# Kernel tuning notes

Measured on AMD Instinct MI355X. Metric: run time of the kernel, lower is better.

The kernel has to match this reference:

```python
import jax, jax.numpy as jnp
import numpy as np

T = 1.0          # temperature
W_PARENT = 0.3
W_CHILD = 0.7
EPS = 1e-8


def _conv(x, w, stride=1):
    # x: [N,C,H,W], w: [O,I,kh,kw]
    return jax.lax.conv_general_dilated(
        x, w, (stride, stride), 'SAME',
        dimension_numbers=('NCHW', 'OIHW', 'NCHW'))


def setup_inputs() -> dict:
    key = jax.random.key(0)
    ks = jax.random.split(key, 12)
    B, H, W = 64, 256, 256
    E, CMID = 8, 8
    GF = 64  # gating feature dim
    s = lambda k, shape, fan: jax.random.normal(k, shape, jnp.float32) * (1.0 / np.sqrt(fan))
    return {
        'x':   jax.random.normal(ks[0], (B, 1, H, W), jnp.float32),
        # gating network (frozen): conv stem + avg pool + two heads
        'Wg':  s(ks[1], (GF, 1, 7, 7), 49),
        'Wc':  s(ks[2], (6, GF), GF),
        'bc':  jnp.zeros((6,), jnp.float32),
        'Wp':  s(ks[3], (2, GF), GF),
        'bp':  jnp.zeros((2,), jnp.float32),
        # 8 experts, each a 1->CMID->1 conv stack (DIVAESR proxy)
        'We1': s(ks[4], (E, CMID, 1, 3, 3), 9),
        'be1': jnp.zeros((E, CMID), jnp.float32),
        'We2': s(ks[5], (E, 1, CMID, 3, 3), 9 * CMID),
        'be2': jnp.zeros((E, 1), jnp.float32),
    }


def _gating(x, Wg, Wc, bc, Wp, bp):
    # frozen multi-task classifier: conv stem, global avg pool, two linear heads
    h = jax.nn.relu(_conv(x, Wg, stride=4))        # [B,GF,H/4,W/4]
    feats = jnp.mean(h, axis=(2, 3))               # [B,GF]
    child_logits = (feats @ Wc.T + bc) / T         # [B,6]
    parent_logits = (feats @ Wp.T + bp) / T        # [B,2]
    child_probs = jax.nn.softmax(child_logits, axis=1)
    parent_probs = jax.nn.softmax(parent_logits, axis=1)
    parent_val = jnp.max(parent_probs, axis=1)
    parent_idx = jnp.argmax(parent_probs, axis=1)
    child_val = jnp.max(child_probs, axis=1)
    child_idx = jnp.argmax(child_probs, axis=1) + 2   # global expert id in [2,7]
    wp = W_PARENT * parent_val
    wc = W_CHILD * child_val
    tot = wp + wc + EPS
    topk_indices = jnp.stack([parent_idx, child_idx], axis=1)   # [B,2] int
    probs = jnp.stack([wp / tot, wc / tot], axis=1)             # [B,2]
    return topk_indices, probs


def _expert_single(xi, w1, b1, w2, b2):
    # xi: [1,H,W]; per-sample expert conv stack with gathered kernels
    h = jax.nn.relu(_conv(xi[None], w1) + b1[None, :, None, None])
    y = _conv(h, w2) + b2[None, :, None, None]
    return y[0]  # [1,H,W]


def _dispatch_combine(x, topk_indices, probs, We1, be1, We2, be2):
    # fused gather-dispatch / combine: gather each sample's two expert kernels
    run = jax.vmap(_expert_single)
    p_idx, c_idx = topk_indices[:, 0], topk_indices[:, 1]
    out_p = run(x, We1[p_idx], be1[p_idx], We2[p_idx], be2[p_idx])  # [B,1,H,W]
    out_c = run(x, We1[c_idx], be1[c_idx], We2[c_idx], be2[c_idx])
    return (probs[:, 0, None, None, None] * out_p
            + probs[:, 1, None, None, None] * out_c)


def reference(x, Wg, Wc, bc, Wp, bp, We1, be1, We2, be2):
    topk_indices, probs = _gating(x, Wg, Wc, bc, Wp, bp)
    return _dispatch_combine(x, topk_indices, probs, We1, be1, We2, be2)
```

## Files before the change

### kernel.cpp

```cpp
#include <hip/hip_runtime.h>
#include <hip/hip_bf16.h>
#include <math.h>

#define IMG 256

typedef __attribute__((ext_vector_type(4))) short short4v;
typedef __attribute__((ext_vector_type(8))) short short8v;
typedef __attribute__((ext_vector_type(4))) float f32x4;
typedef __attribute__((ext_vector_type(2))) float v2f;
typedef _Float16 half2v __attribute__((ext_vector_type(2)));

__device__ __forceinline__ short bf16s(float f) {
    __hip_bfloat16 h = __float2bfloat16(f);
    short s; __builtin_memcpy(&s, &h, 2); return s;
}
__device__ __forceinline__ half2v h2bits(unsigned int u) {
    half2v h; __builtin_memcpy(&h, &u, 4); return h;
}
template <typename T>
__device__ __forceinline__ unsigned int bits4(T v) {
    static_assert(sizeof(T) == 4, "bits4 needs 4-byte type");
    unsigned int u; __builtin_memcpy(&u, &v, 4); return u;
}
__device__ __forceinline__ unsigned int h16b(float f) {
    _Float16 h = (_Float16)f;
    unsigned short s; __builtin_memcpy(&s, &h, 2); return (unsigned int)s;
}

__global__ __launch_bounds__(256) void gate_mfma_kernel(
    const float* __restrict__ x, const float* __restrict__ Wg,
    const float* __restrict__ We2,
    float* __restrict__ partials, unsigned int* __restrict__ w2pack)
{
    __shared__ short xs[36 * 136];
    __shared__ float red[4][64];

    const int tile = blockIdx.x;
    const int rt = tile >> 1, ct = tile & 1;
    const int b   = blockIdx.y;
    const int tid = threadIdx.x;

    const float* xb = x + (size_t)b * (IMG * IMG);
    const int gy0 = rt * 32 - 1;
    {
        const int qx = tid & 31;
        const int rb = tid >> 5;
        #pragma unroll
        for (int t = 0; t < 5; ++t) {
            const int r = rb + 8 * t;
            if (r < 36) {
                const int gy = gy0 + r;
                float4 v = make_float4(0.f, 0.f, 0.f, 0.f);
                if (gy >= 0 && gy < IMG)
                    v = *(const float4*)&xb[gy * IMG + 128 * ct + 4 * qx];
                short* p = &xs[r * 136 + 4 * qx + 1];
                p[0] = bf16s(v.x); p[1] = bf16s(v.y); p[2] = bf16s(v.z); p[3] = bf16s(v.w);
            }
        }
    }
    if (tid < 36) {
        const int r = tid, gy = gy0 + r;
        float v = 0.f;
        if (gy >= 0 && gy < IMG && ct == 1) v = xb[gy * IMG + 127];
        xs[r * 136] = bf16s(v);
    }
    if (tid < 36) {
        const int r = tid, gy = gy0 + r;
        float4 v = make_float4(0.f, 0.f, 0.f, 0.f);
        if (gy >= 0 && gy < IMG && ct == 0)
            v = *(const float4*)&xb[gy * IMG + 128];
        short* p = &xs[r * 136 + 129];
        p[0] = bf16s(v.x); p[1] = bf16s(v.y); p[2] = bf16s(v.z); p[3] = bf16s(v.w);
    }

    const int lane = tid & 63;
    const int wv_  = tid >> 6;
    const int m    = lane & 15;
    const int kb   = lane >> 4;

    short8v Bhi[2][4], Blo[2][4];
    #pragma unroll
    for (int s = 0; s < 2; ++s) {
        const int ky = kb + 4 * s;
        #pragma unroll
        for (int nc = 0; nc < 4; ++nc) {
            const int gf = nc * 16 + m;
            short8v bh, bl;
            #pragma unroll
            for (int j = 0; j < 8; ++j) {
                float wv = 0.f;
                if (j < 7 && ky < 7) wv = Wg[gf * 49 + ky * 7 + j];
                const short hi = bf16s(wv);
                const float hif = __uint_as_float(((unsigned int)(unsigned short)hi) << 16);
                bh[j] = hi;
                bl[j] = bf16s(wv - hif);
            }
            Bhi[s][nc] = bh; Blo[s][nc] = bl;
        }
    }

    __syncthreads();

    float rsum[4] = {0.f, 0.f, 0.f, 0.f};
    const f32x4 zero4 = {0.f, 0.f, 0.f, 0.f};

    #pragma unroll 1
    for (int i = 0; i < 4; ++i) {
        const int chunk = wv_ * 4 + i;
        const int r = chunk >> 1, q = chunk & 1;
        short8v A[2];
        #pragma unroll
        for (int s = 0; s < 2; ++s) {
            const int row = 4 * r + kb + 4 * s;
            const short4v* p = (const short4v*)&xs[row * 136 + 64 * q + 4 * m];
            const short4v lo4 = p[0], hi4 = p[1];
            A[s] = __builtin_shufflevector(lo4, hi4, 0, 1, 2, 3, 4, 5, 6, 7);
        }
        #pragma unroll
        for (int nc = 0; nc < 4; ++nc) {
            f32x4 z = __builtin_amdgcn_mfma_f32_16x16x32_bf16(A[0], Bhi[0][nc], zero4, 0, 0, 0);
            z = __builtin_amdgcn_mfma_f32_16x16x32_bf16(A[1], Bhi[1][nc], z, 0, 0, 0);
            z = __builtin_amdgcn_mfma_f32_16x16x32_bf16(A[0], Blo[0][nc], z, 0, 0, 0);
            z = __builtin_amdgcn_mfma_f32_16x16x32_bf16(A[1], Blo[1][nc], z, 0, 0, 0);
            rsum[nc] += fmaxf(z[0], 0.f) + fmaxf(z[1], 0.f) + fmaxf(z[2], 0.f) + fmaxf(z[3], 0.f);
        }
    }

    #pragma unroll
    for (int nc = 0; nc < 4; ++nc) {
        float v = rsum[nc];
        v += __shfl_xor(v, 16);
        v += __shfl_xor(v, 32);
        if (lane < 16) red[wv_][nc * 16 + lane] = v;
    }
    __syncthreads();
    if (tid < 64) {
        const float s = red[0][tid] + red[1][tid] + red[2][tid] + red[3][tid];
        partials[(b * 16 + tile) * 64 + tid] = s;
    }

    if (tile == 0 && b == 0) {
        for (int i = tid; i < 192; i += 256) {
            const int e = i / 24, rem = i - e * 24;
            const int ch = rem / 3, ky = rem - ch * 3;
            const float* wp = We2 + e * 72 + ch * 9 + ky * 3;
            const unsigned int ha = h16b(wp[0]), hb = h16b(wp[1]), hc = h16b(wp[2]);
            w2pack[i * 4 + 0] = ha | (hb << 16);
            w2pack[i * 4 + 1] = hc;
            w2pack[i * 4 + 2] = (ha << 16);
            w2pack[i * 4 + 3] = hb | (hc << 16);
        }
    }
}

__global__ __launch_bounds__(256) void expert_kernel(
    const float* __restrict__ x,
    const float* __restrict__ We1, const float* __restrict__ be1,
    const unsigned int* __restrict__ w2pack, const float* __restrict__ be2,
    const float* __restrict__ partials,
    const float* __restrict__ Wc, const float* __restrict__ bc,
    const float* __restrict__ Wp, const float* __restrict__ bp,
    float* __restrict__ out)
{
    __shared__ float xs[36 * 40];
    __shared__ __align__(16) unsigned short hs[8 * 34 * 36];
    __shared__ int   gsh_i[2];
    __shared__ float gsh_w[2];

    const int tile = blockIdx.x;
    const int b    = blockIdx.y;
    const int ty = tile >> 3, tx = tile & 7;
    const int y0 = ty * 32, x0 = tx * 32;
    const int tid = threadIdx.x;
    const bool interior = (ty != 0) && (ty != 7) && (tx != 0) && (tx != 7);

    const float* xb = x + (size_t)b * (IMG * IMG);
    if (interior) {
        for (int i = tid; i < 36 * 40; i += 256) {
            int r = i / 40, c = i - r * 40;
            xs[i] = xb[(y0 - 2 + r) * IMG + (x0 - 2 + c)];
        }
    } else {
        for (int i = tid; i < 36 * 40; i += 256) {
            int r = i / 40, c = i - r * 40;
            float v = 0.f;
            if (c < 36) {
                int gy = y0 - 2 + r, gx = x0 - 2 + c;
                if (gy >= 0 && gy < IMG && gx >= 0 && gx < IMG) v = xb[gy * IMG + gx];
            }
            xs[i] = v;
        }
    }

    if (tid < 64) {
        const int g = tid;
        float f = 0.f;
        const float* pb = partials + b * 1024;
        #pragma unroll
        for (int t = 0; t < 16; ++t) f += pb[t * 64 + g];
        f *= (1.0f / 4096.0f);

        float lg[8];
        #pragma unroll
        for (int j = 0; j < 6; ++j) {
            float p = f * Wc[j * 64 + g];
            p += __shfl_xor(p, 1);  p += __shfl_xor(p, 2);  p += __shfl_xor(p, 4);
            p += __shfl_xor(p, 8);  p += __shfl_xor(p, 16); p += __shfl_xor(p, 32);
            lg[j] = p + bc[j];
        }
        #pragma unroll
        for (int j = 0; j < 2; ++j) {
            float p = f * Wp[j * 64 + g];
            p += __shfl_xor(p, 1);  p += __shfl_xor(p, 2);  p += __shfl_xor(p, 4);
            p += __shfl_xor(p, 8);  p += __shfl_xor(p, 16); p += __shfl_xor(p, 32);
            lg[6 + j] = p + bp[j];
        }
        const float pm = fmaxf(lg[6], lg[7]);
        const float e0 = expf(lg[6] - pm), e1 = expf(lg[7] - pm);
        const int   pi = (lg[7] > lg[6]) ? 1 : 0;
        const float pv = fmaxf(e0, e1) / (e0 + e1);
        float cm = lg[0];
        #pragma unroll
        for (int j = 1; j < 6; ++j) cm = fmaxf(cm, lg[j]);
        float es = 0.f, ce[6];
        #pragma unroll
        for (int j = 0; j < 6; ++j) { ce[j] = expf(lg[j] - cm); es += ce[j]; }
        int ci = 0; float cbest = lg[0];
        #pragma unroll
        for (int j = 1; j < 6; ++j) if (lg[j] > cbest) { cbest = lg[j]; ci = j; }
        const float cv = ce[ci] / es;

        const float wpv = 0.3f * pv;
        const float wcv = 0.7f * cv;
        const float tot = wpv + wcv + 1e-8f;
        if (tid == 0) {
            gsh_i[0] = pi;
            gsh_i[1] = ci + 2;
            gsh_w[0] = wpv / tot;
            gsh_w[1] = wcv / tot;
        }
    }

    __syncthreads();

    const int ep = __builtin_amdgcn_readfirstlane(gsh_i[0]);
    const int ec = __builtin_amdgcn_readfirstlane(gsh_i[1]);
    const float wA = __uint_as_float(__builtin_amdgcn_readfirstlane(__float_as_uint(gsh_w[0])));
    const float wB = __uint_as_float(__builtin_amdgcn_readfirstlane(__float_as_uint(gsh_w[1])));

    const int r_ = tid >> 3;
    const int c0 = (tid & 7) << 2;
    const int c1ch   = tid >> 5;
    const int lane32 = tid & 31;

    float oacc0 = 0.f, oacc1 = 0.f, oacc2 = 0.f, oacc3 = 0.f;

    for (int ei = 0; ei < 2; ++ei) {
        const int   e   = ei ? ec : ep;
        const float wgt = ei ? wB : wA;

        float w1r[9];
        const float* w1p = We1 + e * 72 + c1ch * 9;
        #pragma unroll
        for (int k = 0; k < 9; ++k) w1r[k] = w1p[k];
        const float b1r = be1[e * 8 + c1ch];

        if (ei) __syncthreads();

        #pragma unroll 1
        for (int t = 0; t < 3; ++t) {
            const int p = lane32 + 32 * t;
            if (p < 81) {
                const int pr = p / 9;
                const int pc = p - pr * 9;
                const int hy0 = pr << 2;
                const int cb  = pc << 2;

                v2f a01[4], a23[4];
                #pragma unroll
                for (int q = 0; q < 4; ++q) {
                    a01[q] = (v2f){b1r, b1r};
                    a23[q] = (v2f){b1r, b1r};
                }
                #pragma unroll
                for (int r = 0; r < 6; ++r) {
                    const int row = hy0 + r;
                    if (row < 36) {
                        const float* xr = &xs[row * 40 + cb];
                        const v2f P01 = *(const v2f*)(xr);
                        const v2f P23 = *(const v2f*)(xr + 2);
                        const v2f P45 = *(const v2f*)(xr + 4);
                        const v2f P12 = {P01.y, P23.x};
                        const v2f P34 = {P23.y, P45.x};
                        #pragma unroll
                        for (int q = 0; q < 4; ++q) {
                            const int ky = r - q;
                            if (ky >= 0 && ky < 3) {
                                const float wa = w1r[ky * 3 + 0];
                                const float wb = w1r[ky * 3 + 1];
                                const float wcc = w1r[ky * 3 + 2];
                                const v2f wa2 = {wa, wa}, wb2 = {wb, wb}, wc2 = {wcc, wcc};
                                a01[q] = wa2 * P01 + a01[q];
                                a01[q] = wb2 * P12 + a01[q];
                                a01[q] = wc2 * P23 + a01[q];
                                a23[q] = wa2 * P23 + a23[q];
                                a23[q] = wb2 * P34 + a23[q];
                                a23[q] = wc2 * P45 + a23[q];
                            }
                        }
                    }
                }
                if (interior) {
                    #pragma unroll
                    for (int q = 0; q < 4; ++q) {
                        const int hy = hy0 + q;
                        if (hy < 34) {
                            const unsigned int lo = bits4(
                                __builtin_amdgcn_cvt_pkrtz(fmaxf(a01[q].x, 0.f), fmaxf(a01[q].y, 0.f)));
                            const unsigned int hi = bits4(
                                __builtin_amdgcn_cvt_pkrtz(fmaxf(a23[q].x, 0.f), fmaxf(a23[q].y, 0.f)));
                            unsigned short* hp = &hs[c1ch * 1224 + hy * 36 + cb];
                            if (cb < 32) *(uint2*)hp = make_uint2(lo, hi);
                            else         *(unsigned int*)hp = lo;
                        }
                    }
                } else {
                    #pragma unroll
                    for (int q = 0; q < 4; ++q) {
                        const int hy = hy0 + q;
                        if (hy < 34) {
                            const int gy = y0 - 1 + hy;
                            const int gx = x0 - 1 + cb;
                            const bool rowok = (gy >= 0) && (gy < IMG);
                            const float h0 = (rowok && gx >= 0 && gx < IMG) ? fmaxf(a01[q].x, 0.f) : 0.f;
                            const float h1 = (rowok && (gx + 1) < IMG)      ? fmaxf(a01[q].y, 0.f) : 0.f;
                            const float h2 = (rowok && (gx + 2) < IMG)      ? fmaxf(a23[q].x, 0.f) : 0.f;
                            const float h3 = (rowok && (gx + 3) < IMG)      ? fmaxf(a23[q].y, 0.f) : 0.f;
                            const unsigned int lo = bits4(__builtin_amdgcn_cvt_pkrtz(h0, h1));
                            const unsigned int hi = bits4(__builtin_amdgcn_cvt_pkrtz(h2, h3));
                            unsigned short* hp = &hs[c1ch * 1224 + hy * 36 + cb];
                            if (cb < 32) *(uint2*)hp = make_uint2(lo, hi);
                            else         *(unsigned int*)hp = lo;
                        }
                    }
                }
            }
        }
        __syncthreads();

        float a0 = 0.f, a1 = 0.f, a2 = 0.f, a3 = 0.f;
        #pragma unroll
        for (int ch = 0; ch < 8; ++ch) {
            #pragma unroll
            for (int ky = 0; ky < 3; ++ky) {
                const uint4 wp = *(const uint4*)&w2pack[(((e * 8) + ch) * 3 + ky) * 4];
                const unsigned short* hp = &hs[ch * 1224 + (r_ + ky) * 36 + c0];
                const uint2 q4 = *(const uint2*)hp;
                const unsigned int q2 = *(const unsigned int*)(hp + 4);
                const half2v P01 = h2bits(q4.x), P23 = h2bits(q4.y), P45 = h2bits(q2);
                const half2v p0 = h2bits(wp.x), p1 = h2bits(wp.y), p2 = h2bits(wp.z), p3 = h2bits(wp.w);
                a0 = __builtin_amdgcn_fdot2(p0, P01, a0, false);
                a0 = __builtin_amdgcn_fdot2(p1, P23, a0, false);
                a1 = __builtin_amdgcn_fdot2(p2, P01, a1, false);
                a1 = __builtin_amdgcn_fdot2(p3, P23, a1, false);
                a2 = __builtin_amdgcn_fdot2(p0, P23, a2, false);
                a2 = __builtin_amdgcn_fdot2(p1, P45, a2, false);
                a3 = __builtin_amdgcn_fdot2(p2, P23, a3, false);
                a3 = __builtin_amdgcn_fdot2(p3, P45, a3, false);
            }
        }
        const float b2v = be2[e];
        oacc0 += wgt * (a0 + b2v);
        oacc1 += wgt * (a1 + b2v);
        oacc2 += wgt * (a2 + b2v);
        oacc3 += wgt * (a3 + b2v);
    }

    const float4 o4 = make_float4(oacc0, oacc1, oacc2, oacc3);
    *(float4*)&out[(size_t)b * (IMG * IMG) + (y0 + r_) * IMG + (x0 + c0)] = o4;
}

extern "C" void kernel_launch(void* const* d_in, const int* in_sizes, int n_in,
                              void* d_out, int out_size, void* d_ws, size_t ws_size,
                              hipStream_t stream) {
    const float* x   = (const float*)d_in[0];
    const float* Wg  = (const float*)d_in[1];
    const float* Wc  = (const float*)d_in[2];
    const float* bc  = (const float*)d_in[3];
    const float* Wp  = (const float*)d_in[4];
    const float* bp  = (const float*)d_in[5];
    const float* We1 = (const float*)d_in[6];
    const float* be1 = (const float*)d_in[7];
    const float* We2 = (const float*)d_in[8];
    const float* be2 = (const float*)d_in[9];
    float* out = (float*)d_out;

    float*        partials = (float*)d_ws;
    unsigned int* w2pack   = (unsigned int*)((char*)d_ws + 262144);

    gate_mfma_kernel<<<dim3(16, 64), dim3(256), 0, stream>>>(x, Wg, We2, partials, w2pack);
    expert_kernel<<<dim3(64, 64), dim3(256), 0, stream>>>(x, We1, be1, w2pack, be2,
                                                          partials, Wc, bc, Wp, bp, out);
}
```

Baseline: 75.55 us.

## Use 2x2 output micro-tiles in second conv and prefetch gating partials early

Each thread now computes a 2x2 block of outputs instead of a 1x4 row strip in the second expert conv. Rows loaded from shared memory are reused across two output rows, so LDS reads per output drop. The gating partial sums are also loaded into registers before the input tile is staged, to hide their global-load latency. The tradeoffs are more registers and float2 stores in place of float4 stores to the output.

```diff
diff --git a/kernel.cpp b/kernel.cpp
--- a/kernel.cpp
+++ b/kernel.cpp
@@ -174,6 +174,13 @@
     const int tid = threadIdx.x;
     const bool interior = (ty != 0) && (ty != 7) && (tx != 0) && (tx != 7);
 
+    float pacc[16];
+    if (tid < 64) {
+        const float* pb = partials + b * 1024 + tid;
+        #pragma unroll
+        for (int t = 0; t < 16; ++t) pacc[t] = pb[t * 64];
+    }
+
     const float* xb = x + (size_t)b * (IMG * IMG);
     if (interior) {
         for (int i = tid; i < 36 * 40; i += 256) {
@@ -193,12 +200,11 @@
     }
 
     if (tid < 64) {
+        float f = 0.f;
+        #pragma unroll
+        for (int t = 0; t < 16; ++t) f += pacc[t];
+        f *= (1.0f / 4096.0f);
         const int g = tid;
-        float f = 0.f;
-        const float* pb = partials + b * 1024;
-        #pragma unroll
-        for (int t = 0; t < 16; ++t) f += pb[t * 64 + g];
-        f *= (1.0f / 4096.0f);
 
         float lg[8];
         #pragma unroll
@@ -248,12 +254,12 @@
     const float wA = __uint_as_float(__builtin_amdgcn_readfirstlane(__float_as_uint(gsh_w[0])));
     const float wB = __uint_as_float(__builtin_amdgcn_readfirstlane(__float_as_uint(gsh_w[1])));
 
-    const int r_ = tid >> 3;
-    const int c0 = (tid & 7) << 2;
+    const int c2 = tid & 15;
+    const int r2 = tid >> 4;
     const int c1ch   = tid >> 5;
     const int lane32 = tid & 31;
 
-    float oacc0 = 0.f, oacc1 = 0.f, oacc2 = 0.f, oacc3 = 0.f;
+    float oacc00 = 0.f, oacc01 = 0.f, oacc10 = 0.f, oacc11 = 0.f;
 
     for (int ei = 0; ei < 2; ++ei) {
         const int   e   = ei ? ec : ep;
@@ -348,36 +354,69 @@
         }
         __syncthreads();
 
-        float a0 = 0.f, a1 = 0.f, a2 = 0.f, a3 = 0.f;
+        float a00 = 0.f, a01_ = 0.f, a10 = 0.f, a11 = 0.f;
         #pragma unroll
         for (int ch = 0; ch < 8; ++ch) {
-            #pragma unroll
-            for (int ky = 0; ky < 3; ++ky) {
-                const uint4 wp = *(const uint4*)&w2pack[(((e * 8) + ch) * 3 + ky) * 4];
-                const unsigned short* hp = &hs[ch * 1224 + (r_ + ky) * 36 + c0];
-                const uint2 q4 = *(const uint2*)hp;
-                const unsigned int q2 = *(const unsigned int*)(hp + 4);
-                const half2v P01 = h2bits(q4.x), P23 = h2bits(q4.y), P45 = h2bits(q2);
-                const half2v p0 = h2bits(wp.x), p1 = h2bits(wp.y), p2 = h2bits(wp.z), p3 = h2bits(wp.w);
-                a0 = __builtin_amdgcn_fdot2(p0, P01, a0, false);
-                a0 = __builtin_amdgcn_fdot2(p1, P23, a0, false);
-                a1 = __builtin_amdgcn_fdot2(p2, P01, a1, false);
-                a1 = __builtin_amdgcn_fdot2(p3, P23, a1, false);
-                a2 = __builtin_amdgcn_fdot2(p0, P23, a2, false);
-                a2 = __builtin_amdgcn_fdot2(p1, P45, a2, false);
-                a3 = __builtin_amdgcn_fdot2(p2, P23, a3, false);
-                a3 = __builtin_amdgcn_fdot2(p3, P45, a3, false);
+            const uint4 wk0 = *(const uint4*)&w2pack[(((e * 8) + ch) * 3 + 0) * 4];
+            const uint4 wk1 = *(const uint4*)&w2pack[(((e * 8) + ch) * 3 + 1) * 4];
+            const uint4 wk2 = *(const uint4*)&w2pack[(((e * 8) + ch) * 3 + 2) * 4];
+            const unsigned short* hbase = &hs[ch * 1224 + (2 * r2) * 36 + 2 * c2];
+
+            {
+                const unsigned int d0 = *(const unsigned int*)(hbase);
+                const unsigned int d1 = *(const unsigned int*)(hbase + 2);
+                const half2v P01 = h2bits(d0), P23 = h2bits(d1);
+                a00  = __builtin_amdgcn_fdot2(h2bits(wk0.x), P01, a00,  false);
+                a00  = __builtin_amdgcn_fdot2(h2bits(wk0.y), P23, a00,  false);
+                a01_ = __builtin_amdgcn_fdot2(h2bits(wk0.z), P01, a01_, false);
+                a01_ = __builtin_amdgcn_fdot2(h2bits(wk0.w), P23, a01_, false);
+            }
+            {
+                const unsigned int d0 = *(const unsigned int*)(hbase + 36);
+                const unsigned int d1 = *(const unsigned int*)(hbase + 38);
+                const half2v P01 = h2bits(d0), P23 = h2bits(d1);
+                a00  = __builtin_amdgcn_fdot2(h2bits(wk1.x), P01, a00,  false);
+                a00  = __builtin_amdgcn_fdot2(h2bits(wk1.y), P23, a00,  false);
+                a01_ = __builtin_amdgcn_fdot2(h2bits(wk1.z), P01, a01_, false);
+                a01_ = __builtin_amdgcn_fdot2(h2bits(wk1.w), P23, a01_, false);
+                a10  = __builtin_amdgcn_fdot2(h2bits(wk0.x), P01, a10,  false);
+                a10  = __builtin_amdgcn_fdot2(h2bits(wk0.y), P23, a10,  false);
+                a11  = __builtin_amdgcn_fdot2(h2bits(wk0.z), P01, a11,  false);
+                a11  = __builtin_amdgcn_fdot2(h2bits(wk0.w), P23, a11,  false);
+            }
+            {
+                const unsigned int d0 = *(const unsigned int*)(hbase + 72);
+                const unsigned int d1 = *(const unsigned int*)(hbase + 74);
+                const half2v P01 = h2bits(d0), P23 = h2bits(d1);
+                a00  = __builtin_amdgcn_fdot2(h2bits(wk2.x), P01, a00,  false);
+                a00  = __builtin_amdgcn_fdot2(h2bits(wk2.y), P23, a00,  false);
+                a01_ = __builtin_amdgcn_fdot2(h2bits(wk2.z), P01, a01_, false);
+                a01_ = __builtin_amdgcn_fdot2(h2bits(wk2.w), P23, a01_, false);
+                a10  = __builtin_amdgcn_fdot2(h2bits(wk1.x), P01, a10,  false);
+                a10  = __builtin_amdgcn_fdot2(h2bits(wk1.y), P23, a10,  false);
+                a11  = __builtin_amdgcn_fdot2(h2bits(wk1.z), P01, a11,  false);
+                a11  = __builtin_amdgcn_fdot2(h2bits(wk1.w), P23, a11,  false);
+            }
+            {
+                const unsigned int d0 = *(const unsigned int*)(hbase + 108);
+                const unsigned int d1 = *(const unsigned int*)(hbase + 110);
+                const half2v P01 = h2bits(d0), P23 = h2bits(d1);
+                a10 = __builtin_amdgcn_fdot2(h2bits(wk2.x), P01, a10, false);
+                a10 = __builtin_amdgcn_fdot2(h2bits(wk2.y), P23, a10, false);
+                a11 = __builtin_amdgcn_fdot2(h2bits(wk2.z), P01, a11, false);
+                a11 = __builtin_amdgcn_fdot2(h2bits(wk2.w), P23, a11, false);
             }
         }
         const float b2v = be2[e];
-        oacc0 += wgt * (a0 + b2v);
-        oacc1 += wgt * (a1 + b2v);
-        oacc2 += wgt * (a2 + b2v);
-        oacc3 += wgt * (a3 + b2v);
-    }
-
-    const float4 o4 = make_float4(oacc0, oacc1, oacc2, oacc3);
-    *(float4*)&out[(size_t)b * (IMG * IMG) + (y0 + r_) * IMG + (x0 + c0)] = o4;
+        oacc00 += wgt * (a00  + b2v);
+        oacc01 += wgt * (a01_ + b2v);
+        oacc10 += wgt * (a10  + b2v);
+        oacc11 += wgt * (a11  + b2v);
+    }
+
+    float* op = &out[(size_t)b * (IMG * IMG) + (y0 + 2 * r2) * IMG + (x0 + 2 * c2)];
+    *(float2*)op         = make_float2(oacc00, oacc01);
+    *(float2*)(op + IMG) = make_float2(oacc10, oacc11);
 }
 
 extern "C" void kernel_launch(void* const* d_in, const int* in_sizes, int n_in,
```

Result: slower. 77.95 us (+3.2%).
